# Kernel optimization log

Measured on AMD Instinct MI355X. Metric: run time of the kernel, lower is better.

Reference implementation:

```python
import jax, jax.numpy as jnp
import numpy as np

N = 100_000          # nodes
E = 1_600_000        # edges (before self-loops)
D_NODE = 128
D_EDGE = 16
H1, C1 = 8, 8        # conv1: heads=8, out=8 -> concat dim 64
D_EMB = 64           # conv2: heads=1, out=embedding_dim, concat=False
NEG_SLOPE = 0.2      # GATv2 LeakyReLU slope (PyG default)


def _glorot(key, shape, fan):
    return jax.random.normal(key, shape, jnp.float32) * (1.0 / np.sqrt(fan))


def setup_inputs() -> dict:
    key = jax.random.key(0)
    ks = jax.random.split(key, 16)
    return {
        "x": jax.random.normal(ks[0], (N, D_NODE), jnp.float32),
        "edge_index": jax.random.randint(ks[1], (2, E), 0, N, jnp.int64),
        "edge_attr": jax.random.normal(ks[2], (E, D_EDGE), jnp.float32),
        # conv1 params
        "Wl1": _glorot(ks[3], (D_NODE, H1 * C1), D_NODE),
        "bl1": jnp.zeros((H1 * C1,), jnp.float32),
        "Wr1": _glorot(ks[4], (D_NODE, H1 * C1), D_NODE),
        "br1": jnp.zeros((H1 * C1,), jnp.float32),
        "We1": _glorot(ks[5], (D_EDGE, H1 * C1), D_EDGE),
        "att1": _glorot(ks[6], (H1, C1), C1),
        "b1": jnp.zeros((H1 * C1,), jnp.float32),
        # conv2 params (heads=1)
        "Wl2": _glorot(ks[7], (H1 * C1, D_EMB), H1 * C1),
        "bl2": jnp.zeros((D_EMB,), jnp.float32),
        "Wr2": _glorot(ks[8], (H1 * C1, D_EMB), H1 * C1),
        "br2": jnp.zeros((D_EMB,), jnp.float32),
        "We2": _glorot(ks[9], (D_EDGE, D_EMB), D_EDGE),
        "att2": _glorot(ks[10], (1, D_EMB), D_EMB),
        "b2": jnp.zeros((D_EMB,), jnp.float32),
    }


def _add_self_loops(edge_index, edge_attr, n):
    # PyG add_self_loops with fill_value='mean': self-loop edge_attr = mean of
    # incoming edge attrs per destination node.
    src, dst = edge_index[0], edge_index[1]
    ones = jnp.ones((src.shape[0],), edge_attr.dtype)
    deg = jax.ops.segment_sum(ones, dst, num_segments=n)
    ea_mean = jax.ops.segment_sum(edge_attr, dst, num_segments=n)
    ea_mean = ea_mean / jnp.maximum(deg, 1.0)[:, None]
    loop = jnp.arange(n, dtype=src.dtype)
    src2 = jnp.concatenate([src, loop])
    dst2 = jnp.concatenate([dst, loop])
    ea2 = jnp.concatenate([edge_attr, ea_mean], axis=0)
    return src2, dst2, ea2


def _segment_softmax(scores, seg, n):
    # scores: [E, H], seg: [E] destination-node ids
    m = jax.ops.segment_max(scores, seg, num_segments=n)
    m = jnp.where(jnp.isfinite(m), m, 0.0)          # empty segments -> 0
    e = jnp.exp(scores - m[seg])
    s = jax.ops.segment_sum(e, seg, num_segments=n)
    return e / (s[seg] + 1e-16)


def _gatv2(x, src, dst, ea, Wl, bl, Wr, br, We, att, bias, heads, ch, concat):
    n = x.shape[0]
    xl = (x @ Wl + bl).reshape(n, heads, ch)        # W_l x (messages)
    xr = (x @ Wr + br).reshape(n, heads, ch)        # W_r x (queries)
    ee = (ea @ We).reshape(-1, heads, ch)           # edge features
    z = jax.nn.leaky_relu(xl[src] + xr[dst] + ee, NEG_SLOPE)  # [E,H,C]
    score = jnp.einsum('ehc,hc->eh', z, att)
    alpha = _segment_softmax(score, dst, n)         # per-dst softmax
    out = jax.ops.segment_sum(xl[src] * alpha[:, :, None], dst, num_segments=n)
    out = out.reshape(n, heads * ch) if concat else out.mean(axis=1)
    return out + bias


def reference(x, edge_index, edge_attr,
              Wl1, bl1, Wr1, br1, We1, att1, b1,
              Wl2, bl2, Wr2, br2, We2, att2, b2):
    n = x.shape[0]
    src, dst, ea = _add_self_loops(edge_index, edge_attr, n)
    # dropout layers are no-ops in eval mode
    h = jax.nn.elu(_gatv2(x, src, dst, ea, Wl1, bl1, Wr1, br1, We1, att1, b1,
                          H1, C1, True))
    out = _gatv2(h, src, dst, ea, Wl2, bl2, Wr2, br2, We2, att2, b2,
                 1, D_EMB, False)
    return out
```

## Files before the change

kernel.cpp:

```cpp
#include <hip/hip_runtime.h>
#include <hip/hip_bf16.h>

typedef __hip_bfloat16 bf16;

struct Ptrs16 { const void* p[16]; };

__device__ __constant__ int wcnt[14] = {8192,64,8192,64,1024,64,64,4096,64,4096,64,1024,64,64};
__device__ __constant__ int woff[14] = {0,8192,8256,16448,16512,17536,17600,17664,21760,21824,25920,25984,27008,27072};
#define WTOTAL 27136

__global__ void detect_float(Ptrs16 ptrs, int n0, int n1, int* __restrict__ flags)
{
    int b = blockIdx.x, lane = threadIdx.x;
    int count = (b == 0) ? n0 : (b == 1) ? n1 : wcnt[b - 2];
    int limit = count < 1024 ? count : 1024;
    const unsigned short* us = (const unsigned short*)ptrs.p[b];
    int found = 0;
    for (int i = lane; i < limit; i += 64) {
        int e = (us[i] >> 7) & 0xFF;
        if (e >= 143) found = 1;
    }
    unsigned long long any = __ballot(found);
    if (lane == 0) flags[b] = (any != 0ull) ? 0 : 1;
}

__global__ void detect_idx(const int* __restrict__ ei, int* __restrict__ emode)
{
    if (threadIdx.x == 0) {
        int allz = 1;
        for (int i = 0; i < 128; i++)
            if (ei[2 * i + 1] != 0) { allz = 0; break; }
        emode[0] = allz;
    }
}

__global__ __launch_bounds__(256) void convert_weights(
    Ptrs16 ptrs, const int* __restrict__ flags, float* __restrict__ dst)
{
    int i = blockIdx.x * 256 + threadIdx.x;
    if (i >= WTOTAL) return;
    int r = 0;
    while (r < 13 && i >= woff[r + 1]) r++;
    int j = i - woff[r];
    const void* src = ptrs.p[2 + r];
    float v = flags[2 + r] ? __bfloat162float(((const bf16*)src)[j])
                           : ((const float*)src)[j];
    dst[i] = v;
}

__global__ __launch_bounds__(256) void count_kernel(
    const int* __restrict__ ei, int* __restrict__ deg,
    const int* __restrict__ emode, int E, int N)
{
    int e = blockIdx.x * 256 + threadIdx.x;
    if (e >= E) return;
    int stride = 1 + emode[0];
    int d = ei[(E + e) * stride];
    if ((unsigned)d >= (unsigned)N) d = 0;
    atomicAdd(&deg[d], 1);
}

__global__ __launch_bounds__(256) void scan1(
    const int* __restrict__ deg, int* __restrict__ rowptr,
    int* __restrict__ bsum, int N)
{
    __shared__ int ts[256];
    int b = blockIdx.x, t = threadIdx.x;
    int base = b * 1024 + t * 4;
    int v[4]; int s = 0;
#pragma unroll
    for (int i = 0; i < 4; i++) {
        int idx = base + i;
        v[i] = (idx < N) ? deg[idx] : 0;
        s += v[i];
    }
    ts[t] = s;
    __syncthreads();
    for (int off = 1; off < 256; off <<= 1) {
        int x = (t >= off) ? ts[t - off] : 0;
        __syncthreads();
        ts[t] += x;
        __syncthreads();
    }
    int run = (t == 0) ? 0 : ts[t - 1];
#pragma unroll
    for (int i = 0; i < 4; i++) {
        run += v[i];
        int idx = base + i;
        if (idx < N) rowptr[idx + 1] = run;
    }
    if (t == 255) bsum[b] = ts[255];
}

__global__ __launch_bounds__(256) void scan2(int* __restrict__ bsum, int nb)
{
    __shared__ int s[256];
    int t = threadIdx.x;
    s[t] = (t < nb) ? bsum[t] : 0;
    __syncthreads();
    for (int off = 1; off < 256; off <<= 1) {
        int v = (t >= off) ? s[t - off] : 0;
        __syncthreads();
        s[t] += v;
        __syncthreads();
    }
    if (t < nb) bsum[t] = (t == 0) ? 0 : s[t - 1];
}

__global__ __launch_bounds__(256) void scan3(
    int* __restrict__ rowptr, int* __restrict__ fill,
    const int* __restrict__ bsum, int N)
{
    int i = blockIdx.x * 256 + threadIdx.x;
    if (i > N) return;
    int v = (i == 0) ? 0 : rowptr[i] + bsum[(i - 1) >> 10];
    rowptr[i] = v;
    if (i < N) fill[i] = v;
}

__global__ __launch_bounds__(256) void scatter_kernel(
    const int* __restrict__ ei, int* __restrict__ fill,
    const float* __restrict__ ea, float* __restrict__ ea_csr,
    int* __restrict__ src_csr, const int* __restrict__ emode, int E, int N)
{
    int e = blockIdx.x * 256 + threadIdx.x;
    if (e >= E) return;
    int stride = 1 + emode[0];
    int d = ei[(E + e) * stride];
    int s = ei[e * stride];
    if ((unsigned)d >= (unsigned)N) d = 0;
    if ((unsigned)s >= (unsigned)N) s = 0;
    const float4* ea4 = (const float4*)ea;
    float4 v0 = ea4[(long)e * 4 + 0];
    float4 v1 = ea4[(long)e * 4 + 1];
    float4 v2 = ea4[(long)e * 4 + 2];
    float4 v3 = ea4[(long)e * 4 + 3];
    int pos = atomicAdd(&fill[d], 1);
    src_csr[pos] = s;
    float4* dst = (float4*)ea_csr + (long)pos * 4;
    dst[0] = v0; dst[1] = v1; dst[2] = v2; dst[3] = v3;
}

template<int K>
__global__ __launch_bounds__(256) void node_gemm(
    const float* __restrict__ X,
    const float* __restrict__ W0, const float* __restrict__ bias0, float* __restrict__ out0,
    const float* __restrict__ W1, const float* __restrict__ bias1, float* __restrict__ out1,
    int N)
{
    const float* W    = blockIdx.y ? W1 : W0;
    const float* bias = blockIdx.y ? bias1 : bias0;
    float* out        = blockIdx.y ? out1 : out0;

    __shared__ float Ws[K * 64];
    __shared__ float xs[4][4][K];

    for (int idx = threadIdx.x; idx < K * 64; idx += 256)
        Ws[idx] = W[idx];

    int wave = threadIdx.x >> 6, lane = threadIdx.x & 63;
    int r0 = blockIdx.x * 16 + wave * 4;
#pragma unroll
    for (int i = 0; i < 4; i++) {
        int r = r0 + i;
        for (int k = lane; k < K; k += 64)
            xs[wave][i][k] = (r < N) ? X[(long)r * K + k] : 0.0f;
    }
    __syncthreads();

    float a0 = 0.f, a1 = 0.f, a2 = 0.f, a3 = 0.f;
#pragma unroll 4
    for (int k = 0; k < K; k += 4) {
        float4 xv0 = *(const float4*)&xs[wave][0][k];
        float4 xv1 = *(const float4*)&xs[wave][1][k];
        float4 xv2 = *(const float4*)&xs[wave][2][k];
        float4 xv3 = *(const float4*)&xs[wave][3][k];
        float w0 = Ws[(k + 0) * 64 + lane];
        float w1 = Ws[(k + 1) * 64 + lane];
        float w2 = Ws[(k + 2) * 64 + lane];
        float w3 = Ws[(k + 3) * 64 + lane];
        a0 += xv0.x * w0; a1 += xv1.x * w0; a2 += xv2.x * w0; a3 += xv3.x * w0;
        a0 += xv0.y * w1; a1 += xv1.y * w1; a2 += xv2.y * w1; a3 += xv3.y * w1;
        a0 += xv0.z * w2; a1 += xv1.z * w2; a2 += xv2.z * w2; a3 += xv3.z * w2;
        a0 += xv0.w * w3; a1 += xv1.w * w3; a2 += xv2.w * w3; a3 += xv3.w * w3;
    }
    float bz = bias[lane];
    if (r0 + 0 < N) out[(long)(r0 + 0) * 64 + lane] = a0 + bz;
    if (r0 + 1 < N) out[(long)(r0 + 1) * 64 + lane] = a1 + bz;
    if (r0 + 2 < N) out[(long)(r0 + 2) * 64 + lane] = a2 + bz;
    if (r0 + 3 < N) out[(long)(r0 + 3) * 64 + lane] = a3 + bz;
}

#define DPP_ADD(t, ctrl)                                                      \
    t += __int_as_float(__builtin_amdgcn_update_dpp(                          \
             0, __float_as_int(t), (ctrl), 0xF, 0xF, true))

#define DPP_MOV(x, ctrl)                                                      \
    __int_as_float(__builtin_amdgcn_update_dpp(                               \
        0, __float_as_int(x), (ctrl), 0xF, 0xF, true))

template<int CPH>
__device__ __forceinline__ float group_reduce(float t, bool hi4)
{
    if (CPH == 8) {
        DPP_ADD(t, 0xB1);
        DPP_ADD(t, 0x4E);
        float up = DPP_MOV(t, 0x114);
        float dn = DPP_MOV(t, 0x104);
        t += hi4 ? up : dn;
    } else {
        DPP_ADD(t, 0x111);
        DPP_ADD(t, 0x112);
        DPP_ADD(t, 0x114);
        DPP_ADD(t, 0x118);
        DPP_ADD(t, 0x142);
        DPP_ADD(t, 0x143);
        t = __int_as_float(__builtin_amdgcn_readlane(__float_as_int(t), 63));
    }
    return t;
}

template<int CPH, bool FINAL>
__global__ __launch_bounds__(256) void edge_kernel(
    const int* __restrict__ rowptr, const int* __restrict__ src_csr,
    const float* __restrict__ ea_csr,
    const float* __restrict__ xl, const float* __restrict__ xr,
    const float* __restrict__ We, const float* __restrict__ att,
    const float* __restrict__ bias, float* __restrict__ outp, int N)
{
    int lane = threadIdx.x & 63;
    int wave = __builtin_amdgcn_readfirstlane(threadIdx.x >> 6);
    int n = blockIdx.x * 4 + wave;
    if (n >= N) return;

    float wcol[16];
#pragma unroll
    for (int k = 0; k < 16; k++) wcol[k] = We[k * 64 + lane];
    float attc = att[lane];
    float xrc  = xr[(unsigned)n * 64 + lane];
    bool hi4 = (lane & 4) != 0;

    int p0 = __builtin_amdgcn_readfirstlane(rowptr[n]);
    int p1 = __builtin_amdgcn_readfirstlane(rowptr[n + 1]);
    int deg = p1 - p0;

    float l0 = 0.f, acc0 = 0.f, ees0 = 0.f;
    float l1 = 0.f, acc1 = 0.f, ees1 = 0.f;

#define BODY(J, EA_, XS, LL, AC, EE_) do {                                   \
    if (p + (J) < p1) {                                                      \
        float4 a0 = EA_##a, a1 = EA_##b, a2 = EA_##c, a3 = EA_##d;           \
        float xls = XS;                                                      \
        int rp_ = p + (J) + 4; rp_ = (rp_ <= pl) ? rp_ : pl;                 \
        rp_ = __builtin_amdgcn_readfirstlane(rp_);                           \
        EA_##a = g4[(long)rp_ * 4 + 0];                                      \
        EA_##b = g4[(long)rp_ * 4 + 1];                                      \
        EA_##c = g4[(long)rp_ * 4 + 2];                                      \
        EA_##d = g4[(long)rp_ * 4 + 3];                                      \
        int xp_ = p + (J) + 8; xp_ = (xp_ <= pl) ? xp_ : pl;                 \
        int sn_ = __builtin_amdgcn_readfirstlane(src_csr[xp_]);              \
        XS = xl[(unsigned)sn_ * 64 + lane];                                  \
        float t0 = a0.x*wcol[0]  + a0.y*wcol[1];                             \
        float t1 = a0.z*wcol[2]  + a0.w*wcol[3];                             \
        float t2 = a1.x*wcol[4]  + a1.y*wcol[5];                             \
        float t3 = a1.z*wcol[6]  + a1.w*wcol[7];                             \
        float t4 = a2.x*wcol[8]  + a2.y*wcol[9];                             \
        float t5 = a2.z*wcol[10] + a2.w*wcol[11];                            \
        float t6 = a3.x*wcol[12] + a3.y*wcol[13];                            \
        float t7 = a3.z*wcol[14] + a3.w*wcol[15];                            \
        float ee = ((t0 + t1) + (t2 + t3)) + ((t4 + t5) + (t6 + t7));        \
        EE_ += ee;                                                           \
        float z = xls + xrc + ee;                                            \
        z = (z > 0.f) ? z : 0.2f * z;                                        \
        float t = group_reduce<CPH>(z * attc, hi4);                          \
        float pe = __expf(t);                                                \
        LL += pe; AC += pe * xls;                                            \
    } } while (0)

    if (deg > 0) {
        const float4* g4 = (const float4*)ea_csr;
        int pl = p1 - 1;

#define CL(K_) ((p0 + (K_) <= pl) ? p0 + (K_) : pl)
        int q0 = CL(0), q1 = CL(1), q2 = CL(2), q3 = CL(3);
        float4 E0a = g4[(long)q0*4+0], E0b = g4[(long)q0*4+1],
               E0c = g4[(long)q0*4+2], E0d = g4[(long)q0*4+3];
        float4 E1a = g4[(long)q1*4+0], E1b = g4[(long)q1*4+1],
               E1c = g4[(long)q1*4+2], E1d = g4[(long)q1*4+3];
        float4 E2a = g4[(long)q2*4+0], E2b = g4[(long)q2*4+1],
               E2c = g4[(long)q2*4+2], E2d = g4[(long)q2*4+3];
        float4 E3a = g4[(long)q3*4+0], E3b = g4[(long)q3*4+1],
               E3c = g4[(long)q3*4+2], E3d = g4[(long)q3*4+3];
        int s0 = __builtin_amdgcn_readfirstlane(src_csr[CL(0)]);
        int s1 = __builtin_amdgcn_readfirstlane(src_csr[CL(1)]);
        int s2 = __builtin_amdgcn_readfirstlane(src_csr[CL(2)]);
        int s3 = __builtin_amdgcn_readfirstlane(src_csr[CL(3)]);
        int s4 = __builtin_amdgcn_readfirstlane(src_csr[CL(4)]);
        int s5 = __builtin_amdgcn_readfirstlane(src_csr[CL(5)]);
        int s6 = __builtin_amdgcn_readfirstlane(src_csr[CL(6)]);
        int s7 = __builtin_amdgcn_readfirstlane(src_csr[CL(7)]);
#undef CL
        float x0 = xl[(unsigned)s0 * 64 + lane];
        float x1 = xl[(unsigned)s1 * 64 + lane];
        float x2 = xl[(unsigned)s2 * 64 + lane];
        float x3 = xl[(unsigned)s3 * 64 + lane];
        float x4 = xl[(unsigned)s4 * 64 + lane];
        float x5 = xl[(unsigned)s5 * 64 + lane];
        float x6 = xl[(unsigned)s6 * 64 + lane];
        float x7 = xl[(unsigned)s7 * 64 + lane];

        for (int p = p0; p < p1; p += 8) {
            BODY(0, E0, x0, l0, acc0, ees0);
            BODY(1, E1, x1, l1, acc1, ees1);
            BODY(2, E2, x2, l0, acc0, ees0);
            BODY(3, E3, x3, l1, acc1, ees1);
            BODY(4, E0, x4, l0, acc0, ees0);
            BODY(5, E1, x5, l1, acc1, ees1);
            BODY(6, E2, x6, l0, acc0, ees0);
            BODY(7, E3, x7, l1, acc1, ees1);
        }
    }
#undef BODY

    float l = l0 + l1, acc = acc0 + acc1, eeacc = ees0 + ees1;

    {
        float eeS = (deg > 0) ? eeacc / (float)deg : 0.f;
        float xls = xl[(unsigned)n * 64 + lane];
        float z = xls + xrc + eeS;
        z = (z > 0.f) ? z : 0.2f * z;
        float t = group_reduce<CPH>(z * attc, hi4);
        float pe = __expf(t);
        l   += pe;
        acc += pe * xls;
    }

    float out = acc / (l + 1e-16f);
    float v = out + bias[lane];
    if (FINAL) {
        outp[(unsigned)n * 64 + lane] = v;
    } else {
        outp[(unsigned)n * 64 + lane] = (v > 0.f) ? v : (__expf(v) - 1.f);
    }
}

extern "C" void kernel_launch(void* const* d_in, const int* in_sizes, int n_in,
                              void* d_out, int out_size, void* d_ws, size_t ws_size,
                              hipStream_t stream)
{
    const int N = in_sizes[0] / 128;
    const int E = (in_sizes[1] >= 6000000) ? in_sizes[1] / 4 : in_sizes[1] / 2;

    const int*   ei = (const int*)  d_in[1];
    const float* x  = (const float*)d_in[0];
    const float* ea = (const float*)d_in[2];

    Ptrs16 ptrs;
    ptrs.p[0] = d_in[0];
    ptrs.p[1] = d_in[2];
    for (int i = 0; i < 14; i++) ptrs.p[2 + i] = d_in[3 + i];

    char* p = (char*)d_ws;
    auto carve = [&](size_t bytes) {
        char* r = p;
        p += (bytes + 255) & ~(size_t)255;
        return r;
    };
    int*   flags   = (int*)  carve(256);
    int*   emode   = (int*)  carve(256);
    float* wts     = (float*)carve((size_t)WTOTAL * 4);
    int*   deg     = (int*)  carve((size_t)N * 4);
    int*   rowptr  = (int*)  carve((size_t)(N + 1) * 4);
    int*   fill    = (int*)  carve((size_t)N * 4);
    int*   bsum    = (int*)  carve(1024);
    float* xl      = (float*)carve((size_t)N * 64 * 4);
    float* xr      = (float*)carve((size_t)N * 64 * 4);
    float* h       = (float*)carve((size_t)N * 64 * 4);
    float* ea_csr  = (float*)carve((size_t)(E + 32) * 16 * 4);
    int*   src_csr = (int*)  carve((size_t)(E + 32) * 4);
    (void)ws_size; (void)n_in; (void)out_size;

    const float* Wl1f  = wts + 0;     const float* bl1f = wts + 8192;
    const float* Wr1f  = wts + 8256;  const float* br1f = wts + 16448;
    const float* We1f  = wts + 16512; const float* att1f= wts + 17536;
    const float* b1f   = wts + 17600;
    const float* Wl2f  = wts + 17664; const float* bl2f = wts + 21760;
    const float* Wr2f  = wts + 21824; const float* br2f = wts + 25920;
    const float* We2f  = wts + 25984; const float* att2f= wts + 27008;
    const float* b2f   = wts + 27072;

    hipMemsetAsync(deg, 0, (size_t)N * 4, stream);

    detect_float<<<16, 64, 0, stream>>>(ptrs, in_sizes[0], in_sizes[2], flags);
    detect_idx<<<1, 64, 0, stream>>>(ei, emode);
    convert_weights<<<(WTOTAL + 255) / 256, 256, 0, stream>>>(ptrs, flags, wts);

    count_kernel<<<(E + 255) / 256, 256, 0, stream>>>(ei, deg, emode, E, N);

    int nb = (N + 1023) / 1024;
    scan1<<<nb, 256, 0, stream>>>(deg, rowptr, bsum, N);
    scan2<<<1, 256, 0, stream>>>(bsum, nb);
    scan3<<<(N + 256) / 256, 256, 0, stream>>>(rowptr, fill, bsum, N);

    scatter_kernel<<<(E + 255) / 256, 256, 0, stream>>>(
        ei, fill, ea, ea_csr, src_csr, emode, E, N);

    dim3 g1((N + 15) / 16, 2);
    node_gemm<128><<<g1, 256, 0, stream>>>(x, Wl1f, bl1f, xl, Wr1f, br1f, xr, N);
    int ng = (N + 3) / 4;
    edge_kernel<8, false><<<ng, 256, 0, stream>>>(
        rowptr, src_csr, ea_csr, xl, xr, We1f, att1f, b1f, h, N);

    node_gemm<64><<<g1, 256, 0, stream>>>(h, Wl2f, bl2f, xl, Wr2f, br2f, xr, N);
    edge_kernel<64, true><<<ng, 256, 0, stream>>>(
        rowptr, src_csr, ea_csr, xl, xr, We2f, att2f, b2f, (float*)d_out, N);
}
```

Before: 911.5 us.

## Stage edge attributes through LDS and interleave two nodes per wave

The edge kernel now gives each wave two destination nodes and interleaves their per-edge bodies, which adds independent work for latency hiding. Edge attributes for 16 edges are fetched with one coalesced float4 per lane into a per-wave LDS buffer, replacing four uniform-address float4 loads per edge. The next chunk is prefetched while the current one is processed, and the source-feature gathers are prefetched four edges ahead. The cost is more registers and LDS traffic, idle lanes when the two nodes have different degrees, and chunk loads that can read up to 15 edges past a node's range, including past the end of the array for the last node.

```diff
diff --git a/kernel.cpp b/kernel.cpp
--- a/kernel.cpp
+++ b/kernel.cpp
@@ -228,38 +228,70 @@
     const float* __restrict__ We, const float* __restrict__ att,
     const float* __restrict__ bias, float* __restrict__ outp, int N)
 {
+    __shared__ float elds[4][2][256];
+
     int lane = threadIdx.x & 63;
     int wave = __builtin_amdgcn_readfirstlane(threadIdx.x >> 6);
-    int n = blockIdx.x * 4 + wave;
-    if (n >= N) return;
+    int nA = blockIdx.x * 8 + wave * 2;
+    int nB = nA + 1;
+    if (nA >= N) return;
 
     float wcol[16];
 #pragma unroll
     for (int k = 0; k < 16; k++) wcol[k] = We[k * 64 + lane];
     float attc = att[lane];
-    float xrc  = xr[(unsigned)n * 64 + lane];
     bool hi4 = (lane & 4) != 0;
 
-    int p0 = __builtin_amdgcn_readfirstlane(rowptr[n]);
-    int p1 = __builtin_amdgcn_readfirstlane(rowptr[n + 1]);
-    int deg = p1 - p0;
-
-    float l0 = 0.f, acc0 = 0.f, ees0 = 0.f;
-    float l1 = 0.f, acc1 = 0.f, ees1 = 0.f;
-
-#define BODY(J, EA_, XS, LL, AC, EE_) do {                                   \
-    if (p + (J) < p1) {                                                      \
-        float4 a0 = EA_##a, a1 = EA_##b, a2 = EA_##c, a3 = EA_##d;           \
-        float xls = XS;                                                      \
-        int rp_ = p + (J) + 4; rp_ = (rp_ <= pl) ? rp_ : pl;                 \
-        rp_ = __builtin_amdgcn_readfirstlane(rp_);                           \
-        EA_##a = g4[(long)rp_ * 4 + 0];                                      \
-        EA_##b = g4[(long)rp_ * 4 + 1];                                      \
-        EA_##c = g4[(long)rp_ * 4 + 2];                                      \
-        EA_##d = g4[(long)rp_ * 4 + 3];                                      \
-        int xp_ = p + (J) + 8; xp_ = (xp_ <= pl) ? xp_ : pl;                 \
+    int p0A = __builtin_amdgcn_readfirstlane(rowptr[nA]);
+    int p1A = __builtin_amdgcn_readfirstlane(rowptr[nA + 1]);
+    int degA = p1A - p0A, plA = p1A - 1;
+    float xrcA = xr[(unsigned)nA * 64 + lane];
+
+    bool hasB = (nB < N);
+    int p0B = 0, p1B = 0;
+    if (hasB) {
+        p0B = __builtin_amdgcn_readfirstlane(rowptr[nB]);
+        p1B = __builtin_amdgcn_readfirstlane(rowptr[nB + 1]);
+    }
+    int degB = p1B - p0B, plB = p1B - 1;
+    float xrcB = hasB ? xr[(unsigned)nB * 64 + lane] : 0.f;
+
+    float lA = 0.f, accA = 0.f, eesA = 0.f;
+    float lB = 0.f, accB = 0.f, eesB = 0.f;
+
+    const float4* ea4c = (const float4*)ea_csr;
+    float* lbA = &elds[wave][0][0];
+    float* lbB = &elds[wave][1][0];
+
+    float4 nxtA, nxtB;
+    float xA[4], xB[4];
+    if (degA > 0) {
+        nxtA = ea4c[(long)p0A * 4 + lane];
+#pragma unroll
+        for (int k = 0; k < 4; k++) {
+            int i_ = p0A + k; i_ = (i_ <= plA) ? i_ : plA;
+            int s_ = __builtin_amdgcn_readfirstlane(src_csr[i_]);
+            xA[k] = xl[(unsigned)s_ * 64 + lane];
+        }
+    }
+    if (degB > 0) {
+        nxtB = ea4c[(long)p0B * 4 + lane];
+#pragma unroll
+        for (int k = 0; k < 4; k++) {
+            int i_ = p0B + k; i_ = (i_ <= plB) ? i_ : plB;
+            int s_ = __builtin_amdgcn_readfirstlane(src_csr[i_]);
+            xB[k] = xl[(unsigned)s_ * 64 + lane];
+        }
+    }
+
+#define BODYN(I, S) do {                                                     \
+    if (cbase##S + (I) < p1##S) {                                            \
+        const float4* ep_ = (const float4*)(lb##S + (I) * 16);               \
+        float4 a0 = ep_[0], a1 = ep_[1], a2 = ep_[2], a3 = ep_[3];           \
+        float xls = x##S[(I) & 3];                                           \
+        int xp_ = cbase##S + (I) + 4; xp_ = (xp_ <= pl##S) ? xp_ : pl##S;    \
         int sn_ = __builtin_amdgcn_readfirstlane(src_csr[xp_]);              \
-        XS = xl[(unsigned)sn_ * 64 + lane];                                  \
+        x##S[(I) & 3] = xl[(unsigned)sn_ * 64 + lane];                       \
         float t0 = a0.x*wcol[0]  + a0.y*wcol[1];                             \
         float t1 = a0.z*wcol[2]  + a0.w*wcol[3];                             \
         float t2 = a1.x*wcol[4]  + a1.y*wcol[5];                             \
@@ -269,78 +301,74 @@
         float t6 = a3.x*wcol[12] + a3.y*wcol[13];                            \
         float t7 = a3.z*wcol[14] + a3.w*wcol[15];                            \
         float ee = ((t0 + t1) + (t2 + t3)) + ((t4 + t5) + (t6 + t7));        \
-        EE_ += ee;                                                           \
-        float z = xls + xrc + ee;                                            \
+        ees##S += ee;                                                        \
+        float z = xls + xrc##S + ee;                                         \
         z = (z > 0.f) ? z : 0.2f * z;                                        \
         float t = group_reduce<CPH>(z * attc, hi4);                          \
         float pe = __expf(t);                                                \
-        LL += pe; AC += pe * xls;                                            \
+        l##S += pe; acc##S += pe * xls;                                      \
     } } while (0)
 
-    if (deg > 0) {
-        const float4* g4 = (const float4*)ea_csr;
-        int pl = p1 - 1;
-
-#define CL(K_) ((p0 + (K_) <= pl) ? p0 + (K_) : pl)
-        int q0 = CL(0), q1 = CL(1), q2 = CL(2), q3 = CL(3);
-        float4 E0a = g4[(long)q0*4+0], E0b = g4[(long)q0*4+1],
-               E0c = g4[(long)q0*4+2], E0d = g4[(long)q0*4+3];
-        float4 E1a = g4[(long)q1*4+0], E1b = g4[(long)q1*4+1],
-               E1c = g4[(long)q1*4+2], E1d = g4[(long)q1*4+3];
-        float4 E2a = g4[(long)q2*4+0], E2b = g4[(long)q2*4+1],
-               E2c = g4[(long)q2*4+2], E2d = g4[(long)q2*4+3];
-        float4 E3a = g4[(long)q3*4+0], E3b = g4[(long)q3*4+1],
-               E3c = g4[(long)q3*4+2], E3d = g4[(long)q3*4+3];
-        int s0 = __builtin_amdgcn_readfirstlane(src_csr[CL(0)]);
-        int s1 = __builtin_amdgcn_readfirstlane(src_csr[CL(1)]);
-        int s2 = __builtin_amdgcn_readfirstlane(src_csr[CL(2)]);
-        int s3 = __builtin_amdgcn_readfirstlane(src_csr[CL(3)]);
-        int s4 = __builtin_amdgcn_readfirstlane(src_csr[CL(4)]);
-        int s5 = __builtin_amdgcn_readfirstlane(src_csr[CL(5)]);
-        int s6 = __builtin_amdgcn_readfirstlane(src_csr[CL(6)]);
-        int s7 = __builtin_amdgcn_readfirstlane(src_csr[CL(7)]);
-#undef CL
-        float x0 = xl[(unsigned)s0 * 64 + lane];
-        float x1 = xl[(unsigned)s1 * 64 + lane];
-        float x2 = xl[(unsigned)s2 * 64 + lane];
-        float x3 = xl[(unsigned)s3 * 64 + lane];
-        float x4 = xl[(unsigned)s4 * 64 + lane];
-        float x5 = xl[(unsigned)s5 * 64 + lane];
-        float x6 = xl[(unsigned)s6 * 64 + lane];
-        float x7 = xl[(unsigned)s7 * 64 + lane];
-
-        for (int p = p0; p < p1; p += 8) {
-            BODY(0, E0, x0, l0, acc0, ees0);
-            BODY(1, E1, x1, l1, acc1, ees1);
-            BODY(2, E2, x2, l0, acc0, ees0);
-            BODY(3, E3, x3, l1, acc1, ees1);
-            BODY(4, E0, x4, l0, acc0, ees0);
-            BODY(5, E1, x5, l1, acc1, ees1);
-            BODY(6, E2, x6, l0, acc0, ees0);
-            BODY(7, E3, x7, l1, acc1, ees1);
+    int nchA = (degA + 15) >> 4;
+    int nchB = (degB + 15) >> 4;
+    int nch = (nchA > nchB) ? nchA : nchB;
+    for (int ch = 0; ch < nch; ch++) {
+        int cbaseA = p0A + (ch << 4);
+        int cbaseB = p0B + (ch << 4);
+        if (ch < nchA) {
+            ((float4*)lbA)[lane] = nxtA;
+            if (ch + 1 < nchA)
+                nxtA = ea4c[(long)(cbaseA + 16) * 4 + lane];
         }
-    }
-#undef BODY
-
-    float l = l0 + l1, acc = acc0 + acc1, eeacc = ees0 + ees1;
+        if (ch < nchB) {
+            ((float4*)lbB)[lane] = nxtB;
+            if (ch + 1 < nchB)
+                nxtB = ea4c[(long)(cbaseB + 16) * 4 + lane];
+        }
+        BODYN(0,  A); BODYN(0,  B);
+        BODYN(1,  A); BODYN(1,  B);
+        BODYN(2,  A); BODYN(2,  B);
+        BODYN(3,  A); BODYN(3,  B);
+        BODYN(4,  A); BODYN(4,  B);
+        BODYN(5,  A); BODYN(5,  B);
+        BODYN(6,  A); BODYN(6,  B);
+        BODYN(7,  A); BODYN(7,  B);
+        BODYN(8,  A); BODYN(8,  B);
+        BODYN(9,  A); BODYN(9,  B);
+        BODYN(10, A); BODYN(10, B);
+        BODYN(11, A); BODYN(11, B);
+        BODYN(12, A); BODYN(12, B);
+        BODYN(13, A); BODYN(13, B);
+        BODYN(14, A); BODYN(14, B);
+        BODYN(15, A); BODYN(15, B);
+    }
+#undef BODYN
 
     {
-        float eeS = (deg > 0) ? eeacc / (float)deg : 0.f;
-        float xls = xl[(unsigned)n * 64 + lane];
-        float z = xls + xrc + eeS;
+        float eeS = (degA > 0) ? eesA / (float)degA : 0.f;
+        float xls = xl[(unsigned)nA * 64 + lane];
+        float z = xls + xrcA + eeS;
         z = (z > 0.f) ? z : 0.2f * z;
         float t = group_reduce<CPH>(z * attc, hi4);
         float pe = __expf(t);
-        l   += pe;
-        acc += pe * xls;
-    }
-
-    float out = acc / (l + 1e-16f);
-    float v = out + bias[lane];
-    if (FINAL) {
-        outp[(unsigned)n * 64 + lane] = v;
-    } else {
-        outp[(unsigned)n * 64 + lane] = (v > 0.f) ? v : (__expf(v) - 1.f);
+        lA += pe; accA += pe * xls;
+        float out = accA / (lA + 1e-16f);
+        float v = out + bias[lane];
+        if (FINAL) outp[(unsigned)nA * 64 + lane] = v;
+        else       outp[(unsigned)nA * 64 + lane] = (v > 0.f) ? v : (__expf(v) - 1.f);
+    }
+    if (hasB) {
+        float eeS = (degB > 0) ? eesB / (float)degB : 0.f;
+        float xls = xl[(unsigned)nB * 64 + lane];
+        float z = xls + xrcB + eeS;
+        z = (z > 0.f) ? z : 0.2f * z;
+        float t = group_reduce<CPH>(z * attc, hi4);
+        float pe = __expf(t);
+        lB += pe; accB += pe * xls;
+        float out = accB / (lB + 1e-16f);
+        float v = out + bias[lane];
+        if (FINAL) outp[(unsigned)nB * 64 + lane] = v;
+        else       outp[(unsigned)nB * 64 + lane] = (v > 0.f) ? v : (__expf(v) - 1.f);
     }
 }
 
@@ -407,7 +435,7 @@
 
     dim3 g1((N + 15) / 16, 2);
     node_gemm<128><<<g1, 256, 0, stream>>>(x, Wl1f, bl1f, xl, Wr1f, br1f, xr, N);
-    int ng = (N + 3) / 4;
+    int ng = (N + 7) / 8;
     edge_kernel<8, false><<<ng, 256, 0, stream>>>(
         rowptr, src_csr, ea_csr, xl, xr, We1f, att1f, b1f, h, N);
 
```

New measurement: 854.5 us. 6.3% less time.
